# Performance work log

Hardware: AMD Instinct MI355X
Metric: run time of the kernel (lower is better)

Reference implementation:

```python
import jax, jax.numpy as jnp
import numpy as np

P, Q, R = 3, 1, 0          # CliffordAlgebra(p=3, q=1, r=0)
N = P + Q + R
ALG = 1 << N               # 16 basis blades
SHIFTS = (1, 2, 4)


def _cayley():
    """Cayley table C[i,j,k]: blade_i * blade_j = C[i,j,i^j] * blade_{i^j}."""
    metric = [1.0] * P + [-1.0] * Q + [0.0] * R
    C = np.zeros((ALG, ALG, ALG), np.float32)
    for a in range(ALG):
        for b in range(ALG):
            x = a >> 1
            s = 0
            while x:                       # reordering sign
                s += bin(x & b).count('1')
                x >>= 1
            val = -1.0 if (s & 1) else 1.0
            for i in range(N):             # metric for repeated basis vectors
                if (a & b) >> i & 1:
                    val *= metric[i]
            C[a, b, a ^ b] = val
    return C

_C = _cayley()
C0 = jnp.asarray(_C[:, :, 0])                        # grade-0 slice: <a*b>_0
A = jnp.asarray((_C - _C.transpose(1, 0, 2)) / 2.0)  # antisym: (ab - ba)/2
VEC_MASK = jnp.asarray(np.array([1.0 if bin(i).count('1') == 1 else 0.0 for i in range(ALG)], np.float32))
BIV_MASK = jnp.asarray(np.array([1.0 if bin(i).count('1') == 2 else 0.0 for i in range(ALG)], np.float32))


def setup_inputs() -> dict:
    key = jax.random.key(0)
    k1, k2 = jax.random.split(key, 2)
    B, T, D = 8, 4096, 1024
    return {
        "x": jax.random.normal(k1, (B, T, D), jnp.float32),
        "gate_w": jax.random.normal(k2, (D, 1), jnp.float32) * 0.02,
        "gate_b": jnp.zeros((1,), jnp.float32),
        "scalar_weight": jnp.float32(0.5),
        "bivector_weight": jnp.float32(0.5),
    }


def reference(x, gate_w, gate_b, scalar_weight, bivector_weight):
    B, T, D = x.shape
    n = D // ALG                         # 64 chunks of 16 (D divisible, no pad)
    ss = jax.nn.sigmoid(scalar_weight)
    sb = jax.nn.sigmoid(bivector_weight)
    gate = jax.nn.sigmoid(x @ gate_w + gate_b)   # (B,T,1), gate of x (loop-invariant)
    xc = x.reshape(B, T, n, ALG)
    out = x
    for shift in SHIFTS:                 # T=4096 > shift always
        c = x - jnp.roll(x, shift, axis=1)
        cc = c.reshape(B, T, n, ALG)
        # inner product: scalar part per chunk, summed over chunks
        scalar = jnp.einsum('btni,btnj,ij->bt', xc, cc, C0)
        # wedge: antisymmetrized geometric product of vector-grade projections
        av = xc * VEC_MASK
        bv = cc * VEC_MASK
        wedge = jnp.einsum('btni,btnj,ijk->btnk', av, bv, A) * BIV_MASK
        delta = (sb * wedge).reshape(B, T, D)
        delta = delta.at[..., 0].add(ss * scalar)   # scalar_part lives at index 0
        out = out + gate * delta
    return out
```

## Files before the change

### kernel.cpp

```cpp
#include <hip/hip_runtime.h>
#include <math.h>


constexpr int T_DIM   = 4096;
constexpr int D_DIM   = 1024;
constexpr int L_STRIP = 32;
constexpr int NITER   = L_STRIP / 4;
constexpr int NSLOT   = 16;

constexpr int QB0 = 0x8000;
constexpr int QB1 = 0x8055;
constexpr int QB2 = 0x80AA;

template <int PAT>
__device__ __forceinline__ float swz(float v) {
    return __int_as_float(__builtin_amdgcn_ds_swizzle(__float_as_int(v), PAT));
}

__device__ __forceinline__ float sigmoidf(float z) {
    return 1.0f / (1.0f + __expf(-z));
}

__global__ __launch_bounds__(256, 2) void clifford_kernel(
    const float* __restrict__ x,
    const float* __restrict__ gate_w,
    const float* __restrict__ gate_b,
    const float* __restrict__ scalar_w,
    const float* __restrict__ bivec_w,
    float* __restrict__ out,
    int nblocks)
{
    int blk = blockIdx.x;
    if ((gridDim.x & 7) == 0) {
        const int per = gridDim.x >> 3;
        blk = (blockIdx.x & 7) * per + (blockIdx.x >> 3);
    }

    const int tid  = threadIdx.x;
    const int wid  = tid >> 6;
    const int lane = tid & 63;
    const int sub  = lane & 3;
    const int coff = lane << 2;

    const int spb = T_DIM / L_STRIP;
    const int b   = blk / spb;
    const int t0  = (blk - b * spb) * L_STRIP;

    const float* __restrict__ xb = x + (size_t)b * T_DIM * D_DIM;

    __shared__ float ring[NSLOT * D_DIM];

    float4 pa[4], pb[4], st[4], gv[4];
    {
        const int ra = (t0 - 4 + wid) & (T_DIM - 1);
        const int rb = t0 + wid;
        const float* ga = xb + (size_t)ra * D_DIM + coff;
        const float* gs = xb + (size_t)rb * D_DIM + coff;
        #pragma unroll
        for (int m = 0; m < 4; ++m) {
            pa[m] = *(const float4*)(ga + (m << 8));
            pb[m] = *(const float4*)(gs + (m << 8));
            gv[m] = *(const float4*)(gate_w + coff + (m << 8));
        }
        const float* g1 = xb + (size_t)(t0 + 4 + wid) * D_DIM + coff;
        #pragma unroll
        for (int m = 0; m < 4; ++m)
            st[m] = *(const float4*)(g1 + (m << 8));

        float* la = &ring[(wid)     * D_DIM] + coff;
        float* lb = &ring[(wid + 4) * D_DIM] + coff;
        #pragma unroll
        for (int m = 0; m < 4; ++m) {
            *(float4*)(la + (m << 8)) = pa[m];
            *(float4*)(lb + (m << 8)) = pb[m];
        }
    }

    const float ss = sigmoidf(scalar_w[0]);
    const float sb = sigmoidf(bivec_w[0]);
    const float gb = gate_b[0];

    float4 ws;
    if      (sub == 0) ws = make_float4( 1.f,  1.f,  1.f, -1.f);
    else if (sub == 1) ws = make_float4( 1.f, -1.f, -1.f, -1.f);
    else if (sub == 2) ws = make_float4(-1.f,  1.f,  1.f,  1.f);
    else               ws = make_float4( 1.f,  1.f,  1.f, -1.f);
    const float m3  = (sub == 0) ? 1.f : 0.f;
    const float a1  = (sub == 1) ? 1.f : 0.f;
    const float a2  = (sub == 2) ? 1.f : 0.f;
    const float m12 = (sub == 3) ? 1.f : 0.f;

    __syncthreads();

    #pragma unroll
    for (int i = 0; i < NITER; ++i) {
        if (i + 1 < NITER) {
            float* l = &ring[((4 * i + 8 + wid) % NSLOT) * D_DIM] + coff;
            #pragma unroll
            for (int m = 0; m < 4; ++m)
                *(float4*)(l + (m << 8)) = st[m];
        }
        if (i + 2 < NITER) {
            const float* g = xb + (size_t)(t0 + 4 * i + 8 + wid) * D_DIM + coff;
            #pragma unroll
            for (int m = 0; m < 4; ++m)
                st[m] = *(const float4*)(g + (m << 8));
        }

        const int lq = 4 * i + wid + 4;
        const float* rc  = &ring[((lq)          % NSLOT) * D_DIM] + coff;
        const float* rp1 = &ring[((lq - 1)      % NSLOT) * D_DIM] + coff;
        const float* rp2 = &ring[((lq - 2)      % NSLOT) * D_DIM] + coff;
        const float* rp4 = &ring[((lq - 4)      % NSLOT) * D_DIM] + coff;

        float gp = 0.f, sc = 0.f;
        float4 xv[4], dl[4];

        #pragma unroll
        for (int m = 0; m < 4; ++m) {
            xv[m] = *(const float4*)(rc + (m << 8));
            const float4 p1 = *(const float4*)(rp1 + (m << 8));
            const float4 p2 = *(const float4*)(rp2 + (m << 8));
            const float4 p4 = *(const float4*)(rp4 + (m << 8));
            const float4 cur = xv[m];

            float4 cs;
            cs.x = 3.f * cur.x - p1.x - p2.x - p4.x;
            cs.y = 3.f * cur.y - p1.y - p2.y - p4.y;
            cs.z = 3.f * cur.z - p1.z - p2.z - p4.z;
            cs.w = 3.f * cur.w - p1.w - p2.w - p4.w;

            gp += cur.x * gv[m].x + cur.y * gv[m].y
                + cur.z * gv[m].z + cur.w * gv[m].w;
            sc += ws.x * (cur.x * cs.x) + ws.y * (cur.y * cs.y)
                + ws.z * (cur.z * cs.z) + ws.w * (cur.w * cs.w);

            const float x1  = swz<QB0>(cur.y), x2  = swz<QB0>(cur.z);
            const float x4b = swz<QB1>(cur.x), x8b = swz<QB2>(cur.x);
            const float c1  = swz<QB0>(cs.y),  c2  = swz<QB0>(cs.z);
            const float c4b = swz<QB1>(cs.x),  c8b = swz<QB2>(cs.x);

            const float w3  = x1 * c2  - x2  * c1;
            const float w5  = x1 * c4b - x4b * c1;
            const float w6  = x2 * c4b - x4b * c2;
            const float w9  = x1 * c8b - x8b * c1;
            const float w10 = x2 * c8b - x8b * c2;
            const float w12 = x4b * c8b - x8b * c4b;

            dl[m] = make_float4(m12 * w12,
                                a1 * w5 + a2 * w9,
                                a1 * w6 + a2 * w10,
                                m3 * w3);
        }

        #pragma unroll
        for (int o = 32; o > 0; o >>= 1) {
            gp += __shfl_xor(gp, o, 64);
            sc += __shfl_xor(sc, o, 64);
        }
        const float gate = sigmoidf(gp + gb);
        const float gsb  = gate * sb;

        const int t = t0 + 4 * i + wid;
        float* __restrict__ orow = out + ((size_t)b * T_DIM + t) * D_DIM + coff;
        #pragma unroll
        for (int m = 0; m < 4; ++m) {
            float4 o4;
            o4.x = xv[m].x + gsb * dl[m].x;
            o4.y = xv[m].y + gsb * dl[m].y;
            o4.z = xv[m].z + gsb * dl[m].z;
            o4.w = xv[m].w + gsb * dl[m].w;
            if (m == 0 && lane == 0) o4.x += gate * ss * sc;
            *(float4*)(orow + (m << 8)) = o4;
        }

        __syncthreads();
    }
}

extern "C" void kernel_launch(void* const* d_in, const int* in_sizes, int n_in,
                              void* d_out, int out_size, void* d_ws, size_t ws_size,
                              hipStream_t stream) {
    const float* x  = (const float*)d_in[0];
    const float* gw = (const float*)d_in[1];
    const float* gb = (const float*)d_in[2];
    const float* sw = (const float*)d_in[3];
    const float* bw = (const float*)d_in[4];
    float* out = (float*)d_out;

    const int BT      = in_sizes[0] / D_DIM;
    const int nblocks = BT / L_STRIP;
    hipLaunchKernelGGL(clifford_kernel, dim3(nblocks), dim3(256), 0, stream,
                       x, gw, gb, sw, bw, out, nblocks);
}
```

Before: 256.3 us.

## Replace strip-streaming ring with one-shot 4-row blocks using direct global-to-LDS loads

Each block now handles only 4 output rows instead of streaming a 32-row strip through a 16-slot LDS ring. It loads its 8-row window (4 halo rows plus 4 current rows) straight into LDS with global_load_lds, syncs once, and computes. The launch bound is raised to allow 4 blocks per CU. The aim is more parallelism and latency hiding, with register staging and per-iteration barriers removed. The cost is that every row is read twice (once as halo), which doubles read traffic unless neighbouring blocks hit in cache.

```diff
diff --git a/kernel.cpp b/kernel.cpp
--- a/kernel.cpp
+++ b/kernel.cpp
@@ -2,11 +2,10 @@
 #include <math.h>
 
 
-constexpr int T_DIM   = 4096;
-constexpr int D_DIM   = 1024;
-constexpr int L_STRIP = 32;
-constexpr int NITER   = L_STRIP / 4;
-constexpr int NSLOT   = 16;
+constexpr int T_DIM = 4096;
+constexpr int D_DIM = 1024;
+constexpr int NROW  = 4;
+constexpr int NSLOT = 8;
 
 constexpr int QB0 = 0x8000;
 constexpr int QB1 = 0x8055;
@@ -21,7 +20,14 @@
     return 1.0f / (1.0f + __expf(-z));
 }
 
-__global__ __launch_bounds__(256, 2) void clifford_kernel(
+__device__ __forceinline__ void gld16(const float* g, float* l) {
+    __builtin_amdgcn_global_load_lds(
+        (const __attribute__((address_space(1))) unsigned int*)g,
+        (__attribute__((address_space(3))) unsigned int*)l,
+        16, 0, 0);
+}
+
+__global__ __launch_bounds__(256, 4) void clifford_kernel(
     const float* __restrict__ x,
     const float* __restrict__ gate_w,
     const float* __restrict__ gate_b,
@@ -35,6 +41,7 @@
         const int per = gridDim.x >> 3;
         blk = (blockIdx.x & 7) * per + (blockIdx.x >> 3);
     }
+    if (blk >= nblocks) return;
 
     const int tid  = threadIdx.x;
     const int wid  = tid >> 6;
@@ -42,39 +49,29 @@
     const int sub  = lane & 3;
     const int coff = lane << 2;
 
-    const int spb = T_DIM / L_STRIP;
-    const int b   = blk / spb;
-    const int t0  = (blk - b * spb) * L_STRIP;
+    const int rpb = T_DIM / NROW;
+    const int b   = blk / rpb;
+    const int t0  = (blk - b * rpb) * NROW;
 
     const float* __restrict__ xb = x + (size_t)b * T_DIM * D_DIM;
 
     __shared__ float ring[NSLOT * D_DIM];
 
-    float4 pa[4], pb[4], st[4], gv[4];
-    {
-        const int ra = (t0 - 4 + wid) & (T_DIM - 1);
-        const int rb = t0 + wid;
-        const float* ga = xb + (size_t)ra * D_DIM + coff;
-        const float* gs = xb + (size_t)rb * D_DIM + coff;
-        #pragma unroll
-        for (int m = 0; m < 4; ++m) {
-            pa[m] = *(const float4*)(ga + (m << 8));
-            pb[m] = *(const float4*)(gs + (m << 8));
-            gv[m] = *(const float4*)(gate_w + coff + (m << 8));
-        }
-        const float* g1 = xb + (size_t)(t0 + 4 + wid) * D_DIM + coff;
+    #pragma unroll
+    for (int p = 0; p < 2; ++p) {
+        const int q    = p * 4 + wid;
+        const int trow = (t0 + q - 4) & (T_DIM - 1);
+        const float* g = xb + (size_t)trow * D_DIM + coff;
+        float* l       = &ring[q * D_DIM];
         #pragma unroll
         for (int m = 0; m < 4; ++m)
-            st[m] = *(const float4*)(g1 + (m << 8));
+            gld16(g + (m << 8), l + (m << 8));
+    }
 
-        float* la = &ring[(wid)     * D_DIM] + coff;
-        float* lb = &ring[(wid + 4) * D_DIM] + coff;
-        #pragma unroll
-        for (int m = 0; m < 4; ++m) {
-            *(float4*)(la + (m << 8)) = pa[m];
-            *(float4*)(lb + (m << 8)) = pb[m];
-        }
-    }
+    float4 gv[4];
+    #pragma unroll
+    for (int m = 0; m < 4; ++m)
+        gv[m] = *(const float4*)(gate_w + coff + (m << 8));
 
     const float ss = sigmoidf(scalar_w[0]);
     const float sb = sigmoidf(bivec_w[0]);
@@ -92,89 +89,71 @@
 
     __syncthreads();
 
+    const int lq = wid + 4;
+    const float* rc  = &ring[(lq)     * D_DIM] + coff;
+    const float* rp1 = &ring[(lq - 1) * D_DIM] + coff;
+    const float* rp2 = &ring[(lq - 2) * D_DIM] + coff;
+    const float* rp4 = &ring[(lq - 4) * D_DIM] + coff;
+
+    float gp = 0.f, sc = 0.f;
+    float4 xv[4], dl[4];
+
     #pragma unroll
-    for (int i = 0; i < NITER; ++i) {
-        if (i + 1 < NITER) {
-            float* l = &ring[((4 * i + 8 + wid) % NSLOT) * D_DIM] + coff;
-            #pragma unroll
-            for (int m = 0; m < 4; ++m)
-                *(float4*)(l + (m << 8)) = st[m];
-        }
-        if (i + 2 < NITER) {
-            const float* g = xb + (size_t)(t0 + 4 * i + 8 + wid) * D_DIM + coff;
-            #pragma unroll
-            for (int m = 0; m < 4; ++m)
-                st[m] = *(const float4*)(g + (m << 8));
-        }
+    for (int m = 0; m < 4; ++m) {
+        xv[m] = *(const float4*)(rc + (m << 8));
+        const float4 p1 = *(const float4*)(rp1 + (m << 8));
+        const float4 p2 = *(const float4*)(rp2 + (m << 8));
+        const float4 p4 = *(const float4*)(rp4 + (m << 8));
+        const float4 cur = xv[m];
 
-        const int lq = 4 * i + wid + 4;
-        const float* rc  = &ring[((lq)          % NSLOT) * D_DIM] + coff;
-        const float* rp1 = &ring[((lq - 1)      % NSLOT) * D_DIM] + coff;
-        const float* rp2 = &ring[((lq - 2)      % NSLOT) * D_DIM] + coff;
-        const float* rp4 = &ring[((lq - 4)      % NSLOT) * D_DIM] + coff;
+        float4 cs;
+        cs.x = 3.f * cur.x - p1.x - p2.x - p4.x;
+        cs.y = 3.f * cur.y - p1.y - p2.y - p4.y;
+        cs.z = 3.f * cur.z - p1.z - p2.z - p4.z;
+        cs.w = 3.f * cur.w - p1.w - p2.w - p4.w;
 
-        float gp = 0.f, sc = 0.f;
-        float4 xv[4], dl[4];
+        gp += cur.x * gv[m].x + cur.y * gv[m].y
+            + cur.z * gv[m].z + cur.w * gv[m].w;
+        sc += ws.x * (cur.x * cs.x) + ws.y * (cur.y * cs.y)
+            + ws.z * (cur.z * cs.z) + ws.w * (cur.w * cs.w);
 
-        #pragma unroll
-        for (int m = 0; m < 4; ++m) {
-            xv[m] = *(const float4*)(rc + (m << 8));
-            const float4 p1 = *(const float4*)(rp1 + (m << 8));
-            const float4 p2 = *(const float4*)(rp2 + (m << 8));
-            const float4 p4 = *(const float4*)(rp4 + (m << 8));
-            const float4 cur = xv[m];
+        const float x1  = swz<QB0>(cur.y), x2  = swz<QB0>(cur.z);
+        const float x4b = swz<QB1>(cur.x), x8b = swz<QB2>(cur.x);
+        const float c1  = swz<QB0>(cs.y),  c2  = swz<QB0>(cs.z);
+        const float c4b = swz<QB1>(cs.x),  c8b = swz<QB2>(cs.x);
 
-            float4 cs;
-            cs.x = 3.f * cur.x - p1.x - p2.x - p4.x;
-            cs.y = 3.f * cur.y - p1.y - p2.y - p4.y;
-            cs.z = 3.f * cur.z - p1.z - p2.z - p4.z;
-            cs.w = 3.f * cur.w - p1.w - p2.w - p4.w;
+        const float w3  = x1 * c2  - x2  * c1;
+        const float w5  = x1 * c4b - x4b * c1;
+        const float w6  = x2 * c4b - x4b * c2;
+        const float w9  = x1 * c8b - x8b * c1;
+        const float w10 = x2 * c8b - x8b * c2;
+        const float w12 = x4b * c8b - x8b * c4b;
 
-            gp += cur.x * gv[m].x + cur.y * gv[m].y
-                + cur.z * gv[m].z + cur.w * gv[m].w;
-            sc += ws.x * (cur.x * cs.x) + ws.y * (cur.y * cs.y)
-                + ws.z * (cur.z * cs.z) + ws.w * (cur.w * cs.w);
+        dl[m] = make_float4(m12 * w12,
+                            a1 * w5 + a2 * w9,
+                            a1 * w6 + a2 * w10,
+                            m3 * w3);
+    }
 
-            const float x1  = swz<QB0>(cur.y), x2  = swz<QB0>(cur.z);
-            const float x4b = swz<QB1>(cur.x), x8b = swz<QB2>(cur.x);
-            const float c1  = swz<QB0>(cs.y),  c2  = swz<QB0>(cs.z);
-            const float c4b = swz<QB1>(cs.x),  c8b = swz<QB2>(cs.x);
+    #pragma unroll
+    for (int o = 32; o > 0; o >>= 1) {
+        gp += __shfl_xor(gp, o, 64);
+        sc += __shfl_xor(sc, o, 64);
+    }
+    const float gate = sigmoidf(gp + gb);
+    const float gsb  = gate * sb;
 
-            const float w3  = x1 * c2  - x2  * c1;
-            const float w5  = x1 * c4b - x4b * c1;
-            const float w6  = x2 * c4b - x4b * c2;
-            const float w9  = x1 * c8b - x8b * c1;
-            const float w10 = x2 * c8b - x8b * c2;
-            const float w12 = x4b * c8b - x8b * c4b;
-
-            dl[m] = make_float4(m12 * w12,
-                                a1 * w5 + a2 * w9,
-                                a1 * w6 + a2 * w10,
-                                m3 * w3);
-        }
-
-        #pragma unroll
-        for (int o = 32; o > 0; o >>= 1) {
-            gp += __shfl_xor(gp, o, 64);
-            sc += __shfl_xor(sc, o, 64);
-        }
-        const float gate = sigmoidf(gp + gb);
-        const float gsb  = gate * sb;
-
-        const int t = t0 + 4 * i + wid;
-        float* __restrict__ orow = out + ((size_t)b * T_DIM + t) * D_DIM + coff;
-        #pragma unroll
-        for (int m = 0; m < 4; ++m) {
-            float4 o4;
-            o4.x = xv[m].x + gsb * dl[m].x;
-            o4.y = xv[m].y + gsb * dl[m].y;
-            o4.z = xv[m].z + gsb * dl[m].z;
-            o4.w = xv[m].w + gsb * dl[m].w;
-            if (m == 0 && lane == 0) o4.x += gate * ss * sc;
-            *(float4*)(orow + (m << 8)) = o4;
-        }
-
-        __syncthreads();
+    const int t = t0 + wid;
+    float* __restrict__ orow = out + ((size_t)b * T_DIM + t) * D_DIM + coff;
+    #pragma unroll
+    for (int m = 0; m < 4; ++m) {
+        float4 o4;
+        o4.x = xv[m].x + gsb * dl[m].x;
+        o4.y = xv[m].y + gsb * dl[m].y;
+        o4.z = xv[m].z + gsb * dl[m].z;
+        o4.w = xv[m].w + gsb * dl[m].w;
+        if (m == 0 && lane == 0) o4.x += gate * ss * sc;
+        *(float4*)(orow + (m << 8)) = o4;
     }
 }
 
@@ -189,7 +168,7 @@
     float* out = (float*)d_out;
 
     const int BT      = in_sizes[0] / D_DIM;
-    const int nblocks = BT / L_STRIP;
+    const int nblocks = BT / NROW;
     hipLaunchKernelGGL(clifford_kernel, dim3(nblocks), dim3(256), 0, stream,
                        x, gw, gb, sw, bw, out, nblocks);
 }
```

Result: faster. 239.8 us (-6.4%).
